# Optimization experiments

Hardware: AMD Instinct MI355X
Metric: run time of the kernel (lower is better)

Reference implementation:

```python
import jax, jax.numpy as jnp
import numpy as np

B, S, H = 1, 2048, 4096
NH, NKV, HD = 32, 8, 128
MAX_POS, ROPE_THETA = 4096, 10000.0


def setup_inputs() -> dict:
    key = jax.random.key(0)
    ks = jax.random.split(key, 6)
    hidden_states = jax.random.normal(ks[0], (B, S, H), dtype=jnp.float32)
    # additive causal mask (0 on/below diagonal, large negative above)
    causal = jnp.tril(jnp.ones((S, S), dtype=bool))
    attention_mask = jnp.where(causal, 0.0, -1e9).astype(jnp.float32)[None, None]
    position_ids = jnp.broadcast_to(jnp.arange(S, dtype=jnp.int32)[None, :], (B, S))
    sc = 0.02
    Wq = jax.random.normal(ks[1], (H, NH * HD), dtype=jnp.float32) * sc
    Wk = jax.random.normal(ks[2], (H, NKV * HD), dtype=jnp.float32) * sc
    Wv = jax.random.normal(ks[3], (H, NKV * HD), dtype=jnp.float32) * sc
    Wo = jax.random.normal(ks[4], (NH * HD, H), dtype=jnp.float32) * sc
    return {"hidden_states": hidden_states, "attention_mask": attention_mask,
            "position_ids": position_ids, "Wq": Wq, "Wk": Wk, "Wv": Wv, "Wo": Wo}


def _rotate_half(x):
    x1, x2 = x[..., : x.shape[-1] // 2], x[..., x.shape[-1] // 2 :]
    return jnp.concatenate((-x2, x1), axis=-1)


def _rope_tables(seq_len, dtype):
    inv_freq = 1.0 / (ROPE_THETA ** (jnp.arange(0, HD, 2, dtype=jnp.float32) / HD))
    t = jnp.arange(seq_len, dtype=jnp.float32)
    freqs = jnp.einsum("i,j->ij", t, inv_freq)        # [S, HD/2]
    emb = jnp.concatenate((freqs, freqs), axis=-1)     # [S, HD]
    return jnp.cos(emb).astype(dtype), jnp.sin(emb).astype(dtype)


def reference(hidden_states, attention_mask, position_ids, Wq, Wk, Wv, Wo):
    bsz, q_len, _ = hidden_states.shape
    # projections -> [b, h, s, d]
    q = (hidden_states @ Wq).reshape(bsz, q_len, NH, HD).swapaxes(1, 2)
    k = (hidden_states @ Wk).reshape(bsz, q_len, NKV, HD).swapaxes(1, 2)
    v = (hidden_states @ Wv).reshape(bsz, q_len, NKV, HD).swapaxes(1, 2)
    # rotary embedding
    cos, sin = _rope_tables(q_len, hidden_states.dtype)
    cos = jnp.take(cos, position_ids, axis=0)[:, None]  # [b,1,s,d]
    sin = jnp.take(sin, position_ids, axis=0)[:, None]
    q = q * cos + _rotate_half(q) * sin
    k = k * cos + _rotate_half(k) * sin
    # GQA: repeat kv heads
    n_rep = NH // NKV
    k = jnp.repeat(k, n_rep, axis=1)
    v = jnp.repeat(v, n_rep, axis=1)
    # attention
    scores = jnp.einsum("bhqd,bhkd->bhqk", q, k) / jnp.sqrt(jnp.float32(HD)).astype(q.dtype)
    scores = scores + attention_mask
    attn = jax.nn.softmax(scores, axis=-1)
    out = jnp.einsum("bhqk,bhkd->bhqd", attn, v)
    out = out.swapaxes(1, 2).reshape(bsz, q_len, NH * HD)
    return out @ Wo
```

## Files before the change

### kernel.cpp

```cpp
#include <hip/hip_runtime.h>

typedef unsigned short u16;
typedef __attribute__((ext_vector_type(8))) __bf16 bf16x8;
typedef __attribute__((ext_vector_type(4))) __bf16 bf16x4;
typedef __attribute__((ext_vector_type(8))) unsigned short u16x8;
typedef __attribute__((ext_vector_type(4))) unsigned short u16x4;
typedef __attribute__((ext_vector_type(4))) float f32x4;

#define AS1 __attribute__((address_space(1)))
#define AS3 __attribute__((address_space(3)))

__device__ __forceinline__ void load_lds16(const void* g, void* l) {
  __builtin_amdgcn_global_load_lds((const AS1 unsigned int*)g,
                                   (AS3 unsigned int*)l, 16, 0, 0);
}

__device__ __forceinline__ float bf2f(u16 u) {
  unsigned int x = ((unsigned int)u) << 16;
  return __builtin_bit_cast(float, x);
}
__device__ __forceinline__ u16 f2bf(float f) {
  unsigned int x = __builtin_bit_cast(unsigned int, f);
  x += 0x7fffu + ((x >> 16) & 1u);
  return (u16)(x >> 16);
}
__device__ __forceinline__ bf16x8 cvt8(const float* p) {
  f32x4 a = *(const f32x4*)p;
  f32x4 b = *(const f32x4*)(p + 4);
  u16x8 r;
#pragma unroll
  for (int j = 0; j < 4; ++j) { r[j] = f2bf(a[j]); r[4 + j] = f2bf(b[j]); }
  return __builtin_bit_cast(bf16x8, r);
}

__global__ __launch_bounds__(256) void cvt_bf16_kernel(const float* __restrict__ in,
                                                       u16* __restrict__ out) {
  const int i = (blockIdx.x * 256 + threadIdx.x) * 8;
  *(bf16x8*)&out[i] = cvt8(in + i);
}

__global__ __launch_bounds__(256) void transpose_w(const float* __restrict__ in,
                                                   u16* __restrict__ out,
                                                   int R, int C, int col0) {
  __shared__ u16 tile[32][33];
  const int tx = threadIdx.x & 31, ty = threadIdx.x >> 5;
  const int c0 = blockIdx.x * 32, r0 = blockIdx.y * 32;
#pragma unroll
  for (int j = ty; j < 32; j += 8)
    tile[j][tx] = f2bf(in[(size_t)(r0 + j) * C + col0 + c0 + tx]);
  __syncthreads();
#pragma unroll
  for (int j = ty; j < 32; j += 8)
    out[(size_t)(c0 + j) * R + r0 + tx] = tile[tx][j];
}

__device__ __forceinline__ void stage_tile2(const u16* Ag, const u16* Bg,
                                            u16* Asb, u16* Bsb, int w, int K,
                                            int k0) {
#pragma unroll
  for (int j = 0; j < 2; ++j)
    load_lds16(Ag + (size_t)j * 64 * K + k0, Asb + j * 4096 + w * 512);
#pragma unroll
  for (int j = 0; j < 4; ++j)
    load_lds16(Bg + (size_t)j * 64 * K + k0, Bsb + j * 4096 + w * 512);
}

template <int MODE>
__global__ __launch_bounds__(512, 2) void gemm2(const u16* __restrict__ A,
                                                const u16* __restrict__ Bt,
                                                void* __restrict__ Cv,
                                                u16* __restrict__ C2,
                                                int K, int ldC) {
  __shared__ __align__(16) u16 As[3][128 * 64];
  __shared__ __align__(16) u16 Bs[3][256 * 64];
  const int tid = threadIdx.x, lane = tid & 63, w = tid >> 6;
  const int quad = lane >> 4, c16 = lane & 15;

  const int f = blockIdx.y * gridDim.x + blockIdx.x;
  int bm, bn;
  if (gridDim.y == 16) { bn = ((f & 7) * 2 + ((f >> 3) & 1)) * 256; bm = (f >> 4) * 128; }
  else                 { bn = (f & 7) * 256;                        bm = (f >> 3) * 128; }

  const int wm = (w >> 2) * 64, wn = (w & 3) * 64;

  const int l3 = lane >> 3, l7 = lane & 7;
  const int ss = l7 ^ l3;
  const u16* Ag = A + (size_t)(bm + w * 8 + l3) * K + ss * 8;
  const u16* Bg = Bt + (size_t)(bn + w * 8 + l3) * K + ss * 8;
  const int sx = (c16 & 7) << 4;

  f32x4 acc[4][4] = {};
  const int NT = K >> 6;

  stage_tile2(Ag, Bg, As[0], Bs[0], w, K, 0);
  stage_tile2(Ag, Bg, As[1], Bs[1], w, K, 64);
  int bc = 0;
  for (int kt = 0; kt < NT; ++kt) {
    if (kt < NT - 1)
      asm volatile("s_waitcnt vmcnt(6)" ::: "memory");
    else
      asm volatile("s_waitcnt vmcnt(0)" ::: "memory");
    __builtin_amdgcn_s_barrier();
    asm volatile("" ::: "memory");
    const int bp = bc + 2 >= 3 ? bc - 1 : bc + 2;
    if (kt + 2 < NT) stage_tile2(Ag, Bg, As[bp], Bs[bp], w, K, (kt + 2) << 6);

    const u16* Ab = As[bc];
    const u16* Bb = Bs[bc];
    bf16x8 a[4][2], b[4][2];
#pragma unroll
    for (int mt = 0; mt < 4; ++mt)
#pragma unroll
      for (int kc = 0; kc < 2; ++kc) {
        const int row = wm + mt * 16 + c16;
        a[mt][kc] = *(const bf16x8*)&Ab[(row * 128 + ((((kc * 4 + quad) << 4)) ^ sx)) >> 1];
      }
#pragma unroll
    for (int nt = 0; nt < 4; ++nt)
#pragma unroll
      for (int kc = 0; kc < 2; ++kc) {
        const int row = wn + nt * 16 + c16;
        b[nt][kc] = *(const bf16x8*)&Bb[(row * 128 + ((((kc * 4 + quad) << 4)) ^ sx)) >> 1];
      }
    __builtin_amdgcn_s_setprio(1);
#pragma unroll
    for (int kc = 0; kc < 2; ++kc)
#pragma unroll
      for (int mt = 0; mt < 4; ++mt)
#pragma unroll
        for (int nt = 0; nt < 4; ++nt)
          acc[mt][nt] = __builtin_amdgcn_mfma_f32_16x16x32_bf16(a[mt][kc], b[nt][kc], acc[mt][nt], 0, 0, 0);
    __builtin_amdgcn_s_setprio(0);
    bc = bc == 2 ? 0 : bc + 1;
  }
#pragma unroll
  for (int mt = 0; mt < 4; ++mt)
#pragma unroll
    for (int nt = 0; nt < 4; ++nt)
#pragma unroll
      for (int r = 0; r < 4; ++r) {
        const int row = bm + wm + mt * 16 + quad * 4 + r;
        const int col = bn + wn + nt * 16 + c16;
        if (MODE == 1)
          ((float*)Cv)[(size_t)row * ldC + col] = acc[mt][nt][r];
        else if (MODE == 0)
          ((u16*)Cv)[(size_t)row * ldC + col] = f2bf(acc[mt][nt][r]);
        else {
          if (bn < 1024)
            ((u16*)Cv)[(size_t)row * 1024 + col] = f2bf(acc[mt][nt][r]);
          else
            C2[(size_t)(col - 1024) * 2048 + row] = f2bf(acc[mt][nt][r]);
        }
      }
}

__global__ void rope_kernel(u16* __restrict__ buf, const int* __restrict__ pos,
                            int log2nh, float oscale) {
  const int t = blockIdx.x * 256 + threadIdx.x;
  const int i = t & 63;
  const int h = (t >> 6) & ((1 << log2nh) - 1);
  const int s = t >> (6 + log2nh);
  const int nh = 1 << log2nh;
  const float p = (float)pos[s];
  const float invf = exp2f((float)i * -0.20762051915861040f);
  const float ang = p * invf;
  const float cn = cosf(ang), sn = sinf(ang);
  const size_t i1 = (size_t)s * (nh * 128) + h * 128 + i;
  const size_t i2 = i1 + 64;
  const float x1 = bf2f(buf[i1]), x2 = bf2f(buf[i2]);
  buf[i1] = f2bf((x1 * cn - x2 * sn) * oscale);
  buf[i2] = f2bf((x2 * cn + x1 * sn) * oscale);
}

__global__ __launch_bounds__(256, 2) void flash_kernel(const u16* __restrict__ Q,
                                                       const u16* __restrict__ K,
                                                       const u16* __restrict__ VT,
                                                       u16* __restrict__ O) {
  __shared__ __align__(16) u16 Ks[64 * 128];
  __shared__ __align__(16) u16 Vts[128 * 64];
  __shared__ __align__(16) u16 Ps[4][16 * 68];
  const int h = blockIdx.x, kvh = h >> 2;
  const int qb = 31 - blockIdx.y;
  const int tid = threadIdx.x, lane = tid & 63, w = tid >> 6;
  const int quad = lane >> 4, c16 = lane & 15;
  const int rw = lane >> 2, c4 = lane & 3;
  const int sw = (rw & 7) << 3;
  const int sr = (c16 & 7) << 3;

  bf16x8 aq[4];
#pragma unroll
  for (int kc = 0; kc < 4; ++kc)
    aq[kc] = *(const bf16x8*)&Q[(size_t)(qb * 64 + w * 16 + c16) * 4096 + h * 128 + kc * 32 + quad * 8];

  f32x4 acc_o[8] = {};
  float m_run[4], l_run[4];
#pragma unroll
  for (int r = 0; r < 4; ++r) { m_run[r] = -1e30f; l_run[r] = 0.f; }

  bf16x8 kc_[4], vc_[4];
#pragma unroll
  for (int p = 0; p < 4; ++p) {
    kc_[p] = *(const bf16x8*)&K[(size_t)(w * 16 + rw) * 1024 + kvh * 128 + p * 32 + c4 * 8];
    const int d = (p & 1) * 64 + w * 16 + rw;
    vc_[p] = *(const bf16x8*)&VT[(size_t)(kvh * 128 + d) * 2048 + (p >> 1) * 32 + c4 * 8];
  }

  for (int t = 0; t <= qb; ++t) {
    __syncthreads();
    const int key = w * 16 + rw;
#pragma unroll
    for (int p = 0; p < 4; ++p) {
      *(bf16x8*)&Ks[key * 128 + ((p * 32 + c4 * 8) ^ sw)] = kc_[p];
      const int d = (p & 1) * 64 + w * 16 + rw;
      *(bf16x8*)&Vts[d * 64 + ((((p >> 1) * 32 + c4 * 8)) ^ ((d & 7) << 3))] = vc_[p];
    }
    __syncthreads();
    if (t < qb) {
#pragma unroll
      for (int p = 0; p < 4; ++p) {
        kc_[p] = *(const bf16x8*)&K[(size_t)((t + 1) * 64 + w * 16 + rw) * 1024 + kvh * 128 + p * 32 + c4 * 8];
        const int d = (p & 1) * 64 + w * 16 + rw;
        vc_[p] = *(const bf16x8*)&VT[(size_t)(kvh * 128 + d) * 2048 + (t + 1) * 64 + (p >> 1) * 32 + c4 * 8];
      }
    }

    f32x4 sacc[4];
    __builtin_amdgcn_s_setprio(1);
#pragma unroll
    for (int nt = 0; nt < 4; ++nt) {
      f32x4 s = {0.f, 0.f, 0.f, 0.f};
#pragma unroll
      for (int kc = 0; kc < 4; ++kc) {
        bf16x8 bk = *(const bf16x8*)&Ks[(nt * 16 + c16) * 128 + ((kc * 32 + quad * 8) ^ sr)];
        s = __builtin_amdgcn_mfma_f32_16x16x32_bf16(aq[kc], bk, s, 0, 0, 0);
      }
      sacc[nt] = s;
    }
    __builtin_amdgcn_s_setprio(0);
    if (t == qb) {
#pragma unroll
      for (int nt = 0; nt < 4; ++nt)
#pragma unroll
        for (int r = 0; r < 4; ++r)
          if (nt * 16 + c16 > w * 16 + quad * 4 + r) sacc[nt][r] = -1e30f;
    }
    float al[4];
#pragma unroll
    for (int r = 0; r < 4; ++r) {
      float mx = fmaxf(fmaxf(sacc[0][r], sacc[1][r]), fmaxf(sacc[2][r], sacc[3][r]));
#pragma unroll
      for (int off = 1; off < 16; off <<= 1) mx = fmaxf(mx, __shfl_xor(mx, off));
      const float nm = fmaxf(m_run[r], mx);
      al[r] = __expf(m_run[r] - nm);
      m_run[r] = nm;
      float sum = 0.f;
#pragma unroll
      for (int nt = 0; nt < 4; ++nt) {
        const float pv = __expf(sacc[nt][r] - nm);
        sacc[nt][r] = pv;
        sum += pv;
      }
#pragma unroll
      for (int off = 1; off < 16; off <<= 1) sum += __shfl_xor(sum, off);
      l_run[r] = l_run[r] * al[r] + sum;
    }
#pragma unroll
    for (int dt = 0; dt < 8; ++dt)
#pragma unroll
      for (int r = 0; r < 4; ++r) acc_o[dt][r] *= al[r];
#pragma unroll
    for (int nt = 0; nt < 4; ++nt)
#pragma unroll
      for (int r = 0; r < 4; ++r)
        Ps[w][(quad * 4 + r) * 68 + nt * 16 + c16] = f2bf(sacc[nt][r]);
    asm volatile("s_waitcnt lgkmcnt(0)" ::: "memory");
    bf16x8 ap[2];
#pragma unroll
    for (int kc = 0; kc < 2; ++kc) {
      const u16* pp = &Ps[w][c16 * 68 + kc * 32 + quad * 8];
      bf16x4 lo = *(const bf16x4*)pp;
      bf16x4 hi = *(const bf16x4*)(pp + 4);
      bf16x8 apv;
#pragma unroll
      for (int j = 0; j < 4; ++j) { apv[j] = lo[j]; apv[4 + j] = hi[j]; }
      ap[kc] = apv;
    }
    __builtin_amdgcn_s_setprio(1);
#pragma unroll
    for (int dt = 0; dt < 8; ++dt)
#pragma unroll
      for (int kc = 0; kc < 2; ++kc) {
        bf16x8 bv = *(const bf16x8*)&Vts[(dt * 16 + c16) * 64 + ((kc * 32 + quad * 8) ^ sr)];
        acc_o[dt] = __builtin_amdgcn_mfma_f32_16x16x32_bf16(ap[kc], bv, acc_o[dt], 0, 0, 0);
      }
    __builtin_amdgcn_s_setprio(0);
  }
#pragma unroll
  for (int r = 0; r < 4; ++r) {
    const float inv = 1.0f / l_run[r];
    const int row = qb * 64 + w * 16 + quad * 4 + r;
#pragma unroll
    for (int dt = 0; dt < 8; ++dt)
      O[(size_t)row * 4096 + h * 128 + dt * 16 + c16] = f2bf(acc_o[dt][r] * inv);
  }
}

extern "C" void kernel_launch(void* const* d_in, const int* in_sizes, int n_in,
                              void* d_out, int out_size, void* d_ws, size_t ws_size,
                              hipStream_t stream) {
  const float* X  = (const float*)d_in[0];
  const int* pos  = (const int*)d_in[2];
  const float* Wq = (const float*)d_in[3];
  const float* Wk = (const float*)d_in[4];
  const float* Wv = (const float*)d_in[5];
  const float* Wo = (const float*)d_in[6];
  float* out = (float*)d_out;

  const int big = ws_size >= (size_t)50331648;
  char* ws = (char*)d_ws;
  u16* WTq  = (u16*)ws;
  u16* WTkv = (u16*)ws;
  u16* Att, *Xb, *Qb, *Kb, *VTb, *WTo;
  int NPo;
  if (big) {
    Att = (u16*)(ws + 33554432);
    Xb  = Att;
    Qb  = (u16*)d_out;
    Kb  = (u16*)((char*)d_out + 16777216);
    VTb = (u16*)((char*)d_out + 20971520);
    WTo = (u16*)ws;
    NPo = 4096;
  } else {
    Att = (u16*)ws;
    Xb  = (u16*)d_out;
    Qb  = (u16*)((char*)d_out + 16777216);
    Kb  = (u16*)(ws + 16777216);
    VTb = (u16*)(ws + 20971520);
    WTo = (u16*)(ws + 16777216);
    NPo = 2048;
  }

  const dim3 b256(256), b512(512);

  cvt_bf16_kernel<<<dim3(4096), b256, 0, stream>>>(X, Xb);

  transpose_w<<<dim3(128, 128), b256, 0, stream>>>(Wq, WTq, 4096, 4096, 0);
  gemm2<0><<<dim3(16, 16), b512, 0, stream>>>(Xb, WTq, Qb, nullptr, 4096, 4096);

  transpose_w<<<dim3(32, 128), b256, 0, stream>>>(Wk, WTkv, 4096, 1024, 0);
  transpose_w<<<dim3(32, 128), b256, 0, stream>>>(Wv, WTkv + (size_t)1024 * 4096, 4096, 1024, 0);
  gemm2<2><<<dim3(16, 8), b512, 0, stream>>>(Xb, WTkv, Kb, VTb, 4096, 0);

  rope_kernel<<<dim3(2048 * 32 * 64 / 256), b256, 0, stream>>>(Qb, pos, 5, 0.08838834764831845f);
  rope_kernel<<<dim3(2048 * 8 * 64 / 256),  b256, 0, stream>>>(Kb, pos, 3, 1.0f);

  flash_kernel<<<dim3(32, 32), b256, 0, stream>>>(Qb, Kb, VTb, Att);

  for (int p = 0; p < 4096; p += NPo) {
    transpose_w<<<dim3(NPo / 32, 128), b256, 0, stream>>>(Wo, WTo, 4096, 4096, p);
    gemm2<1><<<dim3(16, NPo / 256), b512, 0, stream>>>(Att, WTo, out + p, nullptr, 4096, 4096);
  }
}
```

Measured before the change: 608.0 us.

## Add 128x128-tile double-buffered GEMM for Q and output projections

Introduces gemm3, a 256-thread kernel with 128x128 tiles and two LDS buffers, and uses it for the Q projection and, when the workspace is large, for the output projection. This launches 512 smaller blocks instead of 256 large ones, aiming for better CU fill and occupancy on the many-CU device. gemm2 also drops its swizzled block-to-tile mapping in favour of a plain blockIdx mapping, which may reduce L2 locality for the K/V GEMM. The smaller tiles lower arithmetic intensity per block and have a shallower pipeline than the previous triple-buffered kernel.

```diff
diff --git a/kernel.cpp b/kernel.cpp
--- a/kernel.cpp
+++ b/kernel.cpp
@@ -75,12 +75,7 @@
   __shared__ __align__(16) u16 Bs[3][256 * 64];
   const int tid = threadIdx.x, lane = tid & 63, w = tid >> 6;
   const int quad = lane >> 4, c16 = lane & 15;
-
-  const int f = blockIdx.y * gridDim.x + blockIdx.x;
-  int bm, bn;
-  if (gridDim.y == 16) { bn = ((f & 7) * 2 + ((f >> 3) & 1)) * 256; bm = (f >> 4) * 128; }
-  else                 { bn = (f & 7) * 256;                        bm = (f >> 3) * 128; }
-
+  const int bm = blockIdx.x * 128, bn = blockIdx.y * 256;
   const int wm = (w >> 2) * 64, wn = (w & 3) * 64;
 
   const int l3 = lane >> 3, l7 = lane & 7;
@@ -151,6 +146,84 @@
           else
             C2[(size_t)(col - 1024) * 2048 + row] = f2bf(acc[mt][nt][r]);
         }
+      }
+}
+
+template <int MODE>
+__global__ __launch_bounds__(256, 2) void gemm3(const u16* __restrict__ A,
+                                                const u16* __restrict__ Bt,
+                                                void* __restrict__ Cv,
+                                                int K, int ldC) {
+  __shared__ __align__(16) u16 As[2][128 * 64];
+  __shared__ __align__(16) u16 Bs[2][128 * 64];
+  const int tid = threadIdx.x, lane = tid & 63, w = tid >> 6;
+  const int quad = lane >> 4, c16 = lane & 15;
+  const int bm = blockIdx.x * 128, bn = blockIdx.y * 128;
+  const int wm = (w >> 1) * 64, wn = (w & 1) * 64;
+
+  const int l3 = lane >> 3, l7 = lane & 7;
+  const int ss = l7 ^ l3;
+  const u16* Ag = A + (size_t)(bm + w * 8 + l3) * K + ss * 8;
+  const u16* Bg = Bt + (size_t)(bn + w * 8 + l3) * K + ss * 8;
+  const int sx = (c16 & 7) << 4;
+
+  f32x4 acc[4][4] = {};
+  const int NT = K >> 6;
+
+#define G3_STAGE(buf, k0)                                                   \
+  {                                                                         \
+    _Pragma("unroll") for (int j = 0; j < 4; ++j)                           \
+        load_lds16(Ag + (size_t)j * 32 * K + (k0), As[buf] + j * 2048 + w * 512); \
+    _Pragma("unroll") for (int j = 0; j < 4; ++j)                           \
+        load_lds16(Bg + (size_t)j * 32 * K + (k0), Bs[buf] + j * 2048 + w * 512); \
+  }
+
+  G3_STAGE(0, 0);
+  __syncthreads();
+  for (int kt = 0; kt < NT; ++kt) {
+    const int cur = kt & 1;
+    if (kt + 1 < NT) G3_STAGE(cur ^ 1, (kt + 1) << 6);
+    const u16* Ab = As[cur];
+    const u16* Bb = Bs[cur];
+    bf16x8 a[4][2], b[4][2];
+#pragma unroll
+    for (int mt = 0; mt < 4; ++mt)
+#pragma unroll
+      for (int kc = 0; kc < 2; ++kc) {
+        const int row = wm + mt * 16 + c16;
+        a[mt][kc] = *(const bf16x8*)&Ab[(row * 128 + ((((kc * 4 + quad) << 4)) ^ sx)) >> 1];
+      }
+#pragma unroll
+    for (int nt = 0; nt < 4; ++nt)
+#pragma unroll
+      for (int kc = 0; kc < 2; ++kc) {
+        const int row = wn + nt * 16 + c16;
+        b[nt][kc] = *(const bf16x8*)&Bb[(row * 128 + ((((kc * 4 + quad) << 4)) ^ sx)) >> 1];
+      }
+    __builtin_amdgcn_s_setprio(1);
+#pragma unroll
+    for (int kc = 0; kc < 2; ++kc)
+#pragma unroll
+      for (int mt = 0; mt < 4; ++mt)
+#pragma unroll
+        for (int nt = 0; nt < 4; ++nt)
+          acc[mt][nt] = __builtin_amdgcn_mfma_f32_16x16x32_bf16(a[mt][kc], b[nt][kc], acc[mt][nt], 0, 0, 0);
+    __builtin_amdgcn_s_setprio(0);
+    __syncthreads();
+  }
+#undef G3_STAGE
+#pragma unroll
+  for (int mt = 0; mt < 4; ++mt)
+#pragma unroll
+    for (int nt = 0; nt < 4; ++nt)
+#pragma unroll
+      for (int r = 0; r < 4; ++r) {
+        const int row = bm + wm + mt * 16 + quad * 4 + r;
+        const int col = bn + wn + nt * 16 + c16;
+        if (MODE == 1)
+          ((float*)Cv)[(size_t)row * ldC + col] = acc[mt][nt][r];
+        else
+          ((u16*)Cv)[(size_t)row * ldC + col] = f2bf(acc[mt][nt][r]);
       }
 }
 
@@ -345,7 +418,7 @@
   cvt_bf16_kernel<<<dim3(4096), b256, 0, stream>>>(X, Xb);
 
   transpose_w<<<dim3(128, 128), b256, 0, stream>>>(Wq, WTq, 4096, 4096, 0);
-  gemm2<0><<<dim3(16, 16), b512, 0, stream>>>(Xb, WTq, Qb, nullptr, 4096, 4096);
+  gemm3<0><<<dim3(16, 32), b256, 0, stream>>>(Xb, WTq, Qb, 4096, 4096);
 
   transpose_w<<<dim3(32, 128), b256, 0, stream>>>(Wk, WTkv, 4096, 1024, 0);
   transpose_w<<<dim3(32, 128), b256, 0, stream>>>(Wv, WTkv + (size_t)1024 * 4096, 4096, 1024, 0);
@@ -356,8 +429,13 @@
 
   flash_kernel<<<dim3(32, 32), b256, 0, stream>>>(Qb, Kb, VTb, Att);
 
-  for (int p = 0; p < 4096; p += NPo) {
-    transpose_w<<<dim3(NPo / 32, 128), b256, 0, stream>>>(Wo, WTo, 4096, 4096, p);
-    gemm2<1><<<dim3(16, NPo / 256), b512, 0, stream>>>(Att, WTo, out + p, nullptr, 4096, 4096);
-  }
-}
+  if (big) {
+    transpose_w<<<dim3(128, 128), b256, 0, stream>>>(Wo, WTo, 4096, 4096, 0);
+    gemm3<1><<<dim3(16, 32), b256, 0, stream>>>(Att, WTo, out, 4096, 4096);
+  } else {
+    for (int p = 0; p < 4096; p += NPo) {
+      transpose_w<<<dim3(NPo / 32, 128), b256, 0, stream>>>(Wo, WTo, 4096, 4096, p);
+      gemm2<1><<<dim3(16, NPo / 256), b512, 0, stream>>>(Att, WTo, out + p, nullptr, 4096, 4096);
+    }
+  }
+}
```

After: 577.8 us. -5.0%, faster.
